# Performance work log

Measured on AMD Instinct MI355X. Metric: run time of the kernel, lower is better.

## Reference

```python
import jax, jax.numpy as jnp
import numpy as np

B, S, D = 4, 2048, 1024
P = 2
N_FEAT = 16          # n_feature_know
N_REST = 16          # n_restore_know
R = 128              # knowledge_rank
D_SPACE = 64


def setup_inputs() -> dict:
    key = jax.random.key(0)
    ks = jax.random.split(key, 6)
    x = jax.random.normal(ks[0], (B, S, D), dtype=jnp.float32)
    # per-token routing weights for each of P feature paths, in [0,1)
    feature_paths = jax.random.uniform(ks[1], (P, B, S, N_FEAT), dtype=jnp.float32)
    f_know = jax.random.normal(ks[2], (N_FEAT, D, R), dtype=jnp.float32) * 0.02
    r_know = jax.random.normal(ks[3], (N_REST, R, D), dtype=jnp.float32) * 0.02
    feature_emb = jax.random.normal(ks[4], (N_FEAT, D_SPACE), dtype=jnp.float32)
    W_router = jax.random.normal(ks[5], (D_SPACE + R, N_REST), dtype=jnp.float32) * 0.05
    return {"x": x, "feature_paths": feature_paths, "f_know": f_know,
            "r_know": r_know, "feature_emb": feature_emb, "W_router": W_router}


def reference(x, feature_paths, f_know, r_know, feature_emb, W_router):
    # Feature projection into all N low-rank banks: [B,S,N,R]
    all_h = jnp.einsum('bsd,ndr->bsnr', x, f_know)
    # Weighted sum over banks per path: [P,B,S,R]
    h_all = jnp.einsum('bsnr,pbsn->pbsr', all_h, feature_paths)
    # Context for restore routing: [P,B,S,D_SPACE]
    neuron_ctx = jnp.einsum('pbsn,nd->pbsd', feature_paths, feature_emb)
    # restore_input = cat([neuron_ctx, h]) -> router -> softmax restore weights
    restore_input = jnp.concatenate([neuron_ctx, h_all], axis=-1)  # [P,B,S,D_SPACE+R]
    logits = jnp.einsum('pbsc,cn->pbsn', restore_input, W_router)
    w = jax.nn.softmax(logits, axis=-1)                            # [P,B,S,N_REST]
    # Restore + per-token weighted combine, summed over P paths: [B,S,D]
    output = jnp.einsum('pbsr,nrd,pbsn->bsd', h_all, r_know, w)
    restore_aux_loss = jnp.float32(0.0)
    return output, restore_aux_loss
```

## Files before the change

### kernel.cpp

```cpp
#include <hip/hip_runtime.h>

typedef __attribute__((ext_vector_type(4))) float f32x4;
typedef __bf16 bf16x8 __attribute__((ext_vector_type(8)));
typedef unsigned short ushort_t;

#define T_TOK 8192
#define DIM   1024
#define NRCOL 2048

#define VMW(n)  asm volatile("s_waitcnt vmcnt(" #n ")" ::: "memory")
#define SB0()   __builtin_amdgcn_sched_barrier(0)
#define BAR()   __builtin_amdgcn_s_barrier()

template<int V> struct IC { static constexpr int value = V; };

static __device__ __forceinline__ unsigned short f2bf(float f) {
  unsigned int u = __builtin_bit_cast(unsigned int, f);
  u += 0x7fffu + ((u >> 16) & 1u);
  return (unsigned short)(u >> 16);
}
static __device__ __forceinline__ float bfbits2f(unsigned int lo16) {
  return __builtin_bit_cast(float, lo16 << 16);
}
static __device__ __forceinline__ void gload16(const void* g, void* l) {
  __builtin_amdgcn_global_load_lds((const __attribute__((address_space(1))) void*)g,
                                   (__attribute__((address_space(3))) void*)l, 16, 0, 0);
}

__global__ __launch_bounds__(256) void cvt_f32_bf16(const float* __restrict__ in,
                                                    unsigned short* __restrict__ out,
                                                    int n4) {
  int i = blockIdx.x * 256 + threadIdx.x;
  const int stride = gridDim.x * 256;
  const float4* in4 = (const float4*)in;
  uint2* o4 = (uint2*)out;
  for (; i < n4; i += stride) {
    float4 v = in4[i];
    uint2 o;
    o.x = (unsigned)f2bf(v.x) | ((unsigned)f2bf(v.y) << 16);
    o.y = (unsigned)f2bf(v.z) | ((unsigned)f2bf(v.w) << 16);
    o4[i] = o;
  }
}

__global__ __launch_bounds__(256) void tcvt(const float* __restrict__ src,
                                            unsigned short* __restrict__ dst,
                                            int rows, int cols,
                                            long sstride, long dstride) {
  src += (size_t)blockIdx.z * sstride;
  dst += (size_t)blockIdx.z * dstride;
  __shared__ float tile[32][33];
  const int tx = threadIdx.x & 31, ty = threadIdx.x >> 5;
  const int r0 = blockIdx.y * 32, c0 = blockIdx.x * 32;
  #pragma unroll
  for (int i = 0; i < 32; i += 8)
    tile[ty + i][tx] = src[(size_t)(r0 + ty + i) * cols + c0 + tx];
  __syncthreads();
  #pragma unroll
  for (int i = 0; i < 32; i += 8)
    dst[(size_t)(c0 + ty + i) * rows + r0 + tx] = f2bf(tile[tx][ty + i]);
}

template<int K, bool OUT_BF16>
__global__ __launch_bounds__(512, 2) void gemmT(const ushort_t* __restrict__ A,
                                                const ushort_t* __restrict__ Bt,
                                                void* __restrict__ Cp, int N) {
  constexpr int nt = K >> 6;
  constexpr int NT3 = (nt + 2) / 3;
  __shared__ ushort_t As[3][256 * 64];
  __shared__ ushort_t Bs[3][128 * 64];
  const int tid = threadIdx.x;
  const int nx = gridDim.x;
  const int orig = blockIdx.y * nx + blockIdx.x;
  const int q = (nx * gridDim.y) >> 3;
  const int swz = (orig & 7) * q + (orig >> 3);
  const int bx = swz % nx, by = swz / nx;

  const int lane = tid & 63, wv = tid >> 6;
  const int wm = wv >> 1, wn = wv & 1;
  const int lrow = lane & 15, lk = lane >> 4;

  const ushort_t* Ab = A + (size_t)by * 256 * K;
  const ushort_t* Bb = Bt + (size_t)bx * 128 * K;

  const int rs = tid >> 3;
  const int cs = (tid & 7) ^ (rs & 7);
  const ushort_t* pA[4];
  const ushort_t* pB[2];
  #pragma unroll
  for (int r = 0; r < 4; ++r) pA[r] = Ab + (size_t)(r * 64 + rs) * K + cs * 8;
  #pragma unroll
  for (int r = 0; r < 2; ++r) pB[r] = Bb + (size_t)(r * 64 + rs) * K + cs * 8;
  const int dA = tid * 8;

  int offA[4][2], offB[4][2];
  #pragma unroll
  for (int m = 0; m < 4; ++m) {
    const int ra = wm * 64 + m * 16 + lrow;
    const int rb = wn * 64 + m * 16 + lrow;
    #pragma unroll
    for (int ks = 0; ks < 2; ++ks) {
      offA[m][ks] = ra * 64 + ((ks * 4 + lk) ^ (ra & 7)) * 8;
      offB[m][ks] = rb * 64 + ((ks * 4 + lk) ^ (rb & 7)) * 8;
    }
  }

  f32x4 acc[4][4];
  #pragma unroll
  for (int m = 0; m < 4; ++m)
    #pragma unroll
    for (int n = 0; n < 4; ++n)
      acc[m][n] = (f32x4){0.f, 0.f, 0.f, 0.f};

  #pragma unroll
  for (int r = 0; r < 4; ++r) gload16(pA[r], (void*)&As[0][r * 4096 + dA]);
  #pragma unroll
  for (int r = 0; r < 2; ++r) gload16(pB[r], (void*)&Bs[0][r * 4096 + dA]);
  #pragma unroll
  for (int r = 0; r < 4; ++r) gload16(pA[r] + 64, (void*)&As[1][r * 4096 + dA]);
  #pragma unroll
  for (int r = 0; r < 2; ++r) gload16(pB[r] + 64, (void*)&Bs[1][r * 4096 + dA]);
  #pragma unroll
  for (int r = 0; r < 4; ++r) pA[r] += 128;
  pB[0] += 128; pB[1] += 128;
  VMW(6); SB0(); BAR(); SB0();

  int t = 0;
  auto body = [&](auto SC) {
    constexpr int S = SC.value;
    constexpr int S2 = (S + 2) % 3;
    if (t >= nt) return;
    bf16x8 av[4][2], bv[4][2];
    #pragma unroll
    for (int m = 0; m < 4; ++m)
      #pragma unroll
      for (int ks = 0; ks < 2; ++ks) {
        av[m][ks] = *(const bf16x8*)&As[S][offA[m][ks]];
        bv[m][ks] = *(const bf16x8*)&Bs[S][offB[m][ks]];
      }
    if (t + 2 < nt) {
      #pragma unroll
      for (int r = 0; r < 4; ++r) gload16(pA[r], (void*)&As[S2][r * 4096 + dA]);
      #pragma unroll
      for (int r = 0; r < 2; ++r) gload16(pB[r], (void*)&Bs[S2][r * 4096 + dA]);
    }
    __builtin_amdgcn_s_setprio(1);
    #pragma unroll
    for (int ks = 0; ks < 2; ++ks)
      #pragma unroll
      for (int m = 0; m < 4; ++m)
        #pragma unroll
        for (int n = 0; n < 4; ++n)
          acc[m][n] = __builtin_amdgcn_mfma_f32_16x16x32_bf16(av[m][ks], bv[n][ks], acc[m][n], 0, 0, 0);
    __builtin_amdgcn_s_setprio(0);
    SB0();
    if (t + 2 < nt) { VMW(6); } else { VMW(0); }
    SB0(); BAR(); SB0();
    #pragma unroll
    for (int r = 0; r < 4; ++r) pA[r] += 64;
    pB[0] += 64; pB[1] += 64;
    ++t;
  };
  #pragma unroll 1
  for (int i = 0; i < NT3; ++i) {
    body(IC<0>{}); body(IC<1>{}); body(IC<2>{});
  }

  #pragma unroll
  for (int m = 0; m < 4; ++m) {
    const int row0 = by * 256 + wm * 64 + m * 16 + lk * 4;
    #pragma unroll
    for (int n = 0; n < 4; ++n) {
      const int col = bx * 128 + wn * 64 + n * 16 + lrow;
      #pragma unroll
      for (int j = 0; j < 4; ++j) {
        const size_t idx = (size_t)(row0 + j) * N + col;
        if constexpr (OUT_BF16) ((ushort_t*)Cp)[idx] = f2bf(acc[m][n][j]);
        else                    ((float*)Cp)[idx] = acc[m][n][j];
      }
    }
  }
}

__global__ __launch_bounds__(256) void middle_kernel(const unsigned short* __restrict__ AH,
                                                     const float* __restrict__ fp,
                                                     const float* __restrict__ femb,
                                                     const float* __restrict__ Wr,
                                                     unsigned short* __restrict__ Mout,
                                                     float* __restrict__ auxout) {
  __shared__ float G[16][16];
  __shared__ float hs[4][2][128];
  __shared__ float wsm[4][2][16];
  const int tid = threadIdx.x;
  {
    const int n = tid >> 4, j = tid & 15;
    float s = 0.f;
    #pragma unroll
    for (int ds = 0; ds < 64; ++ds) s += femb[n * 64 + ds] * Wr[ds * 16 + j];
    G[n][j] = s;
  }
  const int wv = tid >> 6, l = tid & 63;
  const int t = blockIdx.x * 4 + wv;

  float p0[16], p1[16];
  #pragma unroll
  for (int n = 0; n < 16; ++n) {
    p0[n] = fp[t * 16 + n];
    p1[n] = fp[T_TOK * 16 + t * 16 + n];
  }

  float h00 = 0.f, h01 = 0.f, h10 = 0.f, h11 = 0.f;
  const unsigned short* ahrow = AH + (size_t)t * NRCOL;
  #pragma unroll
  for (int n = 0; n < 16; ++n) {
    const unsigned int v = *(const unsigned int*)(ahrow + n * 128 + 2 * l);
    const float a0 = bfbits2f(v & 0xffffu);
    const float a1 = bfbits2f(v >> 16);
    h00 += a0 * p0[n]; h01 += a1 * p0[n];
    h10 += a0 * p1[n]; h11 += a1 * p1[n];
  }
  hs[wv][0][2 * l] = h00; hs[wv][0][2 * l + 1] = h01;
  hs[wv][1][2 * l] = h10; hs[wv][1][2 * l + 1] = h11;
  __syncthreads();

  if (l < 32) {
    const int p = l >> 4, j = l & 15;
    float s = 0.f;
    #pragma unroll
    for (int n = 0; n < 16; ++n) s += (p ? p1[n] : p0[n]) * G[n][j];
    const float* hp = hs[wv][p];
    const float* wr = Wr + 64 * 16 + j;
    float s0 = 0.f, s1 = 0.f, s2 = 0.f, s3 = 0.f;
    #pragma unroll
    for (int r = 0; r < 128; r += 4) {
      s0 += hp[r]     * wr[(r)     * 16];
      s1 += hp[r + 1] * wr[(r + 1) * 16];
      s2 += hp[r + 2] * wr[(r + 2) * 16];
      s3 += hp[r + 3] * wr[(r + 3) * 16];
    }
    s += (s0 + s1) + (s2 + s3);
    float mx = s;
    #pragma unroll
    for (int d = 1; d < 16; d <<= 1) mx = fmaxf(mx, __shfl_xor(mx, d, 64));
    const float e = __expf(s - mx);
    float sum = e;
    #pragma unroll
    for (int d = 1; d < 16; d <<= 1) sum += __shfl_xor(sum, d, 64);
    wsm[wv][p][j] = e / sum;
  }
  __syncthreads();

  unsigned short* mrow = Mout + (size_t)t * NRCOL;
  #pragma unroll
  for (int n = 0; n < 16; ++n) {
    const float w0 = wsm[wv][0][n], w1 = wsm[wv][1][n];
    const float m0 = w0 * h00 + w1 * h10;
    const float m1 = w0 * h01 + w1 * h11;
    const unsigned int pk = (unsigned)f2bf(m0) | ((unsigned)f2bf(m1) << 16);
    *(unsigned int*)(mrow + n * 128 + 2 * l) = pk;
  }
  if (blockIdx.x == 0 && tid == 0) auxout[0] = 0.f;
}

extern "C" void kernel_launch(void* const* d_in, const int* in_sizes, int n_in,
                              void* d_out, int out_size, void* d_ws, size_t ws_size,
                              hipStream_t stream) {
  const float* x    = (const float*)d_in[0];
  const float* fp   = (const float*)d_in[1];
  const float* fk   = (const float*)d_in[2];
  const float* rk   = (const float*)d_in[3];
  const float* femb = (const float*)d_in[4];
  const float* Wr   = (const float*)d_in[5];
  float* out = (float*)d_out;

  char* ws = (char*)d_ws;
  unsigned short* Xbf = (unsigned short*)ws;
  unsigned short* W1t = (unsigned short*)(ws + 16u * 1024 * 1024);
  unsigned short* Mb  = (unsigned short*)ws;
  unsigned short* W2t = (unsigned short*)(ws + 32u * 1024 * 1024);
  unsigned short* AH  = (unsigned short*)(ws + 36u * 1024 * 1024);

  cvt_f32_bf16<<<2048, 256, 0, stream>>>(x, Xbf, (T_TOK * DIM) / 4);
  tcvt<<<dim3(128 / 32, 1024 / 32, 16), 256, 0, stream>>>(fk, W1t, 1024, 128,
                                                          1024L * 128, 128L * 1024);
  tcvt<<<dim3(1024 / 32, 2048 / 32, 1), 256, 0, stream>>>(rk, W2t, 2048, 1024, 0, 0);
  gemmT<1024, true><<<dim3(NRCOL / 128, T_TOK / 256), 512, 0, stream>>>(Xbf, W1t, AH, NRCOL);
  middle_kernel<<<T_TOK / 4, 256, 0, stream>>>(AH, fp, femb, Wr, Mb, out + 8388608);
  gemmT<2048, false><<<dim3(DIM / 128, T_TOK / 256), 512, 0, stream>>>(Mb, W2t, out, DIM);
}
```

Before: 124.4 us.

## Restructure GEMM with parameterized tiles, register double-buffering and split MFMA phases

Replaces the fixed 256x128 GEMM with a templated kernel that takes BM and BK and uses a 256-wide N tile and a 2x4 wave layout. Each k-step is split into two MFMA halves so the LDS fragment reads for the next stage overlap the current compute, and the A fragments are double-buffered in registers. The first GEMM uses 256x256 tiles with BK=32 and the second uses 128x256 tiles with BK=64. This trades more registers, a fully unrolled k-loop and an extra barrier per step for more operand reuse and better overlap of LDS reads with MFMA work.

```diff
diff --git a/kernel.cpp b/kernel.cpp
--- a/kernel.cpp
+++ b/kernel.cpp
@@ -11,8 +11,6 @@
 #define VMW(n)  asm volatile("s_waitcnt vmcnt(" #n ")" ::: "memory")
 #define SB0()   __builtin_amdgcn_sched_barrier(0)
 #define BAR()   __builtin_amdgcn_s_barrier()
-
-template<int V> struct IC { static constexpr int value = V; };
 
 static __device__ __forceinline__ unsigned short f2bf(float f) {
   unsigned int u = __builtin_bit_cast(unsigned int, f);
@@ -61,14 +59,20 @@
     dst[(size_t)(c0 + ty + i) * rows + r0 + tx] = f2bf(tile[tx][ty + i]);
 }
 
-template<int K, bool OUT_BF16>
-__global__ __launch_bounds__(512, 2) void gemmT(const ushort_t* __restrict__ A,
+template<int BM, int BK, int K, bool OUT_BF16>
+__global__ __launch_bounds__(512, 2) void gemmP(const ushort_t* __restrict__ A,
                                                 const ushort_t* __restrict__ Bt,
                                                 void* __restrict__ Cp, int N) {
-  constexpr int nt = K >> 6;
-  constexpr int NT3 = (nt + 2) / 3;
-  __shared__ ushort_t As[3][256 * 64];
-  __shared__ ushort_t Bs[3][128 * 64];
+  constexpr int nt = K / BK;
+  constexpr int KS = BK / 32;
+  constexpr int MF = BM / 32;
+  constexpr int CH = BK / 8;
+  constexpr int AR = BM * BK * 2 / 8192;
+  constexpr int BR = 256 * BK * 2 / 8192;
+  constexpr int LPT = AR + BR;
+  __shared__ ushort_t As[3][BM * BK];
+  __shared__ ushort_t Bs[3][256 * BK];
+
   const int tid = threadIdx.x;
   const int nx = gridDim.x;
   const int orig = blockIdx.y * nx + blockIdx.x;
@@ -77,101 +81,115 @@
   const int bx = swz % nx, by = swz / nx;
 
   const int lane = tid & 63, wv = tid >> 6;
-  const int wm = wv >> 1, wn = wv & 1;
+  const int wm = wv >> 2, wn = wv & 3;
   const int lrow = lane & 15, lk = lane >> 4;
 
-  const ushort_t* Ab = A + (size_t)by * 256 * K;
-  const ushort_t* Bb = Bt + (size_t)bx * 128 * K;
-
-  const int rs = tid >> 3;
-  const int cs = (tid & 7) ^ (rs & 7);
-  const ushort_t* pA[4];
-  const ushort_t* pB[2];
-  #pragma unroll
-  for (int r = 0; r < 4; ++r) pA[r] = Ab + (size_t)(r * 64 + rs) * K + cs * 8;
-  #pragma unroll
-  for (int r = 0; r < 2; ++r) pB[r] = Bb + (size_t)(r * 64 + rs) * K + cs * 8;
-  const int dA = tid * 8;
-
-  int offA[4][2], offB[4][2];
-  #pragma unroll
-  for (int m = 0; m < 4; ++m) {
-    const int ra = wm * 64 + m * 16 + lrow;
-    const int rb = wn * 64 + m * 16 + lrow;
-    #pragma unroll
-    for (int ks = 0; ks < 2; ++ks) {
-      offA[m][ks] = ra * 64 + ((ks * 4 + lk) ^ (ra & 7)) * 8;
-      offB[m][ks] = rb * 64 + ((ks * 4 + lk) ^ (rb & 7)) * 8;
-    }
-  }
-
-  f32x4 acc[4][4];
-  #pragma unroll
-  for (int m = 0; m < 4; ++m)
+  const ushort_t* Ab = A + (size_t)by * BM * K;
+  const ushort_t* Bb = Bt + (size_t)bx * 256 * K;
+
+  const int srow = tid * 16 / (BK * 2);
+  const int sch = ((tid * 16 >> 4) & (CH - 1)) ^ (srow & (CH - 1));
+  constexpr int RPR = 8192 / (BK * 2);
+  const ushort_t* pA[AR];
+  const ushort_t* pB[BR];
+  #pragma unroll
+  for (int r = 0; r < AR; ++r) pA[r] = Ab + (size_t)(r * RPR + srow) * K + sch * 8;
+  #pragma unroll
+  for (int r = 0; r < BR; ++r) pB[r] = Bb + (size_t)(r * RPR + srow) * K + sch * 8;
+  const int dL = tid * 8;
+
+  int oA[MF], oB[4];
+  #pragma unroll
+  for (int m = 0; m < MF; ++m) {
+    const int r = wm * (BM / 2) + m * 16 + lrow;
+    oA[m] = r * BK + (lk ^ (r & (CH - 1))) * 8;
+  }
+  #pragma unroll
+  for (int n = 0; n < 4; ++n) {
+    const int r = wn * 64 + n * 16 + lrow;
+    oB[n] = r * BK + (lk ^ (r & (CH - 1))) * 8;
+  }
+
+  f32x4 acc[MF][4];
+  #pragma unroll
+  for (int m = 0; m < MF; ++m)
     #pragma unroll
     for (int n = 0; n < 4; ++n)
       acc[m][n] = (f32x4){0.f, 0.f, 0.f, 0.f};
 
-  #pragma unroll
-  for (int r = 0; r < 4; ++r) gload16(pA[r], (void*)&As[0][r * 4096 + dA]);
-  #pragma unroll
-  for (int r = 0; r < 2; ++r) gload16(pB[r], (void*)&Bs[0][r * 4096 + dA]);
-  #pragma unroll
-  for (int r = 0; r < 4; ++r) gload16(pA[r] + 64, (void*)&As[1][r * 4096 + dA]);
-  #pragma unroll
-  for (int r = 0; r < 2; ++r) gload16(pB[r] + 64, (void*)&Bs[1][r * 4096 + dA]);
-  #pragma unroll
-  for (int r = 0; r < 4; ++r) pA[r] += 128;
-  pB[0] += 128; pB[1] += 128;
-  VMW(6); SB0(); BAR(); SB0();
-
-  int t = 0;
-  auto body = [&](auto SC) {
-    constexpr int S = SC.value;
-    constexpr int S2 = (S + 2) % 3;
-    if (t >= nt) return;
-    bf16x8 av[4][2], bv[4][2];
-    #pragma unroll
-    for (int m = 0; m < 4; ++m)
-      #pragma unroll
-      for (int ks = 0; ks < 2; ++ks) {
-        av[m][ks] = *(const bf16x8*)&As[S][offA[m][ks]];
-        bv[m][ks] = *(const bf16x8*)&Bs[S][offB[m][ks]];
-      }
-    if (t + 2 < nt) {
-      #pragma unroll
-      for (int r = 0; r < 4; ++r) gload16(pA[r], (void*)&As[S2][r * 4096 + dA]);
-      #pragma unroll
-      for (int r = 0; r < 2; ++r) gload16(pB[r], (void*)&Bs[S2][r * 4096 + dA]);
+  auto stage = [&](int s, int adv) {
+    #pragma unroll
+    for (int r = 0; r < AR; ++r) gload16(pA[r] + adv, (void*)&As[s][r * 4096 + dL]);
+    #pragma unroll
+    for (int r = 0; r < BR; ++r) gload16(pB[r] + adv, (void*)&Bs[s][r * 4096 + dL]);
+  };
+
+  stage(0, 0);
+  stage(1, BK);
+  if constexpr (LPT == 4) VMW(4); else VMW(6);
+  SB0(); BAR(); SB0();
+
+  bf16x8 av[2][MF][KS], bv01[2][KS], bv23[2][KS];
+  #pragma unroll
+  for (int m = 0; m < MF; ++m)
+    #pragma unroll
+    for (int ks = 0; ks < KS; ++ks)
+      av[0][m][ks] = *(const bf16x8*)&As[0][oA[m] ^ (ks * 32)];
+  #pragma unroll
+  for (int n = 0; n < 2; ++n)
+    #pragma unroll
+    for (int ks = 0; ks < KS; ++ks)
+      bv01[n][ks] = *(const bf16x8*)&Bs[0][oB[n] ^ (ks * 32)];
+
+  #pragma unroll
+  for (int t = 0; t < nt; ++t) {
+    const int s = t % 3, s1 = (t + 1) % 3, s2 = (t + 2) % 3;
+    const int p = t & 1;
+    if (t + 2 < nt) stage(s2, (t + 2) * BK);
+    #pragma unroll
+    for (int n = 0; n < 2; ++n)
+      #pragma unroll
+      for (int ks = 0; ks < KS; ++ks)
+        bv23[n][ks] = *(const bf16x8*)&Bs[s][oB[n + 2] ^ (ks * 32)];
+    #pragma unroll
+    for (int ks = 0; ks < KS; ++ks)
+      #pragma unroll
+      for (int m = 0; m < MF; ++m)
+        #pragma unroll
+        for (int n = 0; n < 2; ++n)
+          acc[m][n] = __builtin_amdgcn_mfma_f32_16x16x32_bf16(av[p][m][ks], bv01[n][ks], acc[m][n], 0, 0, 0);
+    SB0();
+    if (t + 2 < nt) { if constexpr (LPT == 4) VMW(4); else VMW(6); }
+    else            { VMW(0); }
+    BAR(); SB0();
+    if (t + 1 < nt) {
+      #pragma unroll
+      for (int m = 0; m < MF; ++m)
+        #pragma unroll
+        for (int ks = 0; ks < KS; ++ks)
+          av[p ^ 1][m][ks] = *(const bf16x8*)&As[s1][oA[m] ^ (ks * 32)];
+      #pragma unroll
+      for (int n = 0; n < 2; ++n)
+        #pragma unroll
+        for (int ks = 0; ks < KS; ++ks)
+          bv01[n][ks] = *(const bf16x8*)&Bs[s1][oB[n] ^ (ks * 32)];
     }
-    __builtin_amdgcn_s_setprio(1);
-    #pragma unroll
-    for (int ks = 0; ks < 2; ++ks)
-      #pragma unroll
-      for (int m = 0; m < 4; ++m)
+    #pragma unroll
+    for (int ks = 0; ks < KS; ++ks)
+      #pragma unroll
+      for (int m = 0; m < MF; ++m)
         #pragma unroll
-        for (int n = 0; n < 4; ++n)
-          acc[m][n] = __builtin_amdgcn_mfma_f32_16x16x32_bf16(av[m][ks], bv[n][ks], acc[m][n], 0, 0, 0);
-    __builtin_amdgcn_s_setprio(0);
-    SB0();
-    if (t + 2 < nt) { VMW(6); } else { VMW(0); }
+        for (int n = 0; n < 2; ++n)
+          acc[m][n + 2] = __builtin_amdgcn_mfma_f32_16x16x32_bf16(av[p][m][ks], bv23[n][ks], acc[m][n + 2], 0, 0, 0);
     SB0(); BAR(); SB0();
-    #pragma unroll
-    for (int r = 0; r < 4; ++r) pA[r] += 64;
-    pB[0] += 64; pB[1] += 64;
-    ++t;
-  };
-  #pragma unroll 1
-  for (int i = 0; i < NT3; ++i) {
-    body(IC<0>{}); body(IC<1>{}); body(IC<2>{});
-  }
-
-  #pragma unroll
-  for (int m = 0; m < 4; ++m) {
-    const int row0 = by * 256 + wm * 64 + m * 16 + lk * 4;
+  }
+
+  #pragma unroll
+  for (int m = 0; m < MF; ++m) {
+    const int row0 = by * BM + wm * (BM / 2) + m * 16 + lk * 4;
     #pragma unroll
     for (int n = 0; n < 4; ++n) {
-      const int col = bx * 128 + wn * 64 + n * 16 + lrow;
+      const int col = bx * 256 + wn * 64 + n * 16 + lrow;
       #pragma unroll
       for (int j = 0; j < 4; ++j) {
         const size_t idx = (size_t)(row0 + j) * N + col;
@@ -284,7 +302,7 @@
   tcvt<<<dim3(128 / 32, 1024 / 32, 16), 256, 0, stream>>>(fk, W1t, 1024, 128,
                                                           1024L * 128, 128L * 1024);
   tcvt<<<dim3(1024 / 32, 2048 / 32, 1), 256, 0, stream>>>(rk, W2t, 2048, 1024, 0, 0);
-  gemmT<1024, true><<<dim3(NRCOL / 128, T_TOK / 256), 512, 0, stream>>>(Xbf, W1t, AH, NRCOL);
+  gemmP<256, 32, 1024, true><<<dim3(NRCOL / 256, T_TOK / 256), 512, 0, stream>>>(Xbf, W1t, AH, NRCOL);
   middle_kernel<<<T_TOK / 4, 256, 0, stream>>>(AH, fp, femb, Wr, Mb, out + 8388608);
-  gemmT<2048, false><<<dim3(DIM / 128, T_TOK / 256), 512, 0, stream>>>(Mb, W2t, out, DIM);
-}
+  gemmP<128, 64, 2048, false><<<dim3(DIM / 256, T_TOK / 128), 512, 0, stream>>>(Mb, W2t, out, DIM);
+}
```

After: 115.9 us. 6.9% less time.

## Switch GEMMs to 32x32x16 MFMA with 128x256 tiles and full unrolling

Applied to the files above, without the earlier changes.

Rewrites the bf16 GEMM kernel to use 32x32x16 MFMA instructions instead of 16x16x32, with a 128x256 block tile (A rows x B rows) and a 2x4 wave layout where each wave computes 64x64 from 2x2 MFMA tiles. The K loop is fully unrolled with compile-time stage indices, and the LDS swizzle is adapted to the new fragment layout. The larger MFMA shape needs fewer LDS fragment reads per flop and fewer instructions, at the cost of more register pressure from full unrolling and a different, more strided store pattern in the epilogue.

```diff
diff --git a/kernel.cpp b/kernel.cpp
--- a/kernel.cpp
+++ b/kernel.cpp
@@ -1,6 +1,6 @@
 #include <hip/hip_runtime.h>
 
-typedef __attribute__((ext_vector_type(4))) float f32x4;
+typedef __attribute__((ext_vector_type(16))) float f32x16;
 typedef __bf16 bf16x8 __attribute__((ext_vector_type(8)));
 typedef unsigned short ushort_t;
 
@@ -11,8 +11,6 @@
 #define VMW(n)  asm volatile("s_waitcnt vmcnt(" #n ")" ::: "memory")
 #define SB0()   __builtin_amdgcn_sched_barrier(0)
 #define BAR()   __builtin_amdgcn_s_barrier()
-
-template<int V> struct IC { static constexpr int value = V; };
 
 static __device__ __forceinline__ unsigned short f2bf(float f) {
   unsigned int u = __builtin_bit_cast(unsigned int, f);
@@ -62,13 +60,13 @@
 }
 
 template<int K, bool OUT_BF16>
-__global__ __launch_bounds__(512, 2) void gemmT(const ushort_t* __restrict__ A,
-                                                const ushort_t* __restrict__ Bt,
-                                                void* __restrict__ Cp, int N) {
-  constexpr int nt = K >> 6;
-  constexpr int NT3 = (nt + 2) / 3;
-  __shared__ ushort_t As[3][256 * 64];
-  __shared__ ushort_t Bs[3][128 * 64];
+__global__ __launch_bounds__(512, 2) void gemm32(const ushort_t* __restrict__ A,
+                                                 const ushort_t* __restrict__ Bt,
+                                                 void* __restrict__ Cp, int N) {
+  constexpr int nt = K / 64;
+  __shared__ ushort_t As[3][128 * 64];
+  __shared__ ushort_t Bs[3][256 * 64];
+
   const int tid = threadIdx.x;
   const int nx = gridDim.x;
   const int orig = blockIdx.y * nx + blockIdx.x;
@@ -77,104 +75,92 @@
   const int bx = swz % nx, by = swz / nx;
 
   const int lane = tid & 63, wv = tid >> 6;
-  const int wm = wv >> 1, wn = wv & 1;
-  const int lrow = lane & 15, lk = lane >> 4;
-
-  const ushort_t* Ab = A + (size_t)by * 256 * K;
-  const ushort_t* Bb = Bt + (size_t)bx * 128 * K;
-
-  const int rs = tid >> 3;
-  const int cs = (tid & 7) ^ (rs & 7);
-  const ushort_t* pA[4];
-  const ushort_t* pB[2];
-  #pragma unroll
-  for (int r = 0; r < 4; ++r) pA[r] = Ab + (size_t)(r * 64 + rs) * K + cs * 8;
-  #pragma unroll
-  for (int r = 0; r < 2; ++r) pB[r] = Bb + (size_t)(r * 64 + rs) * K + cs * 8;
-  const int dA = tid * 8;
-
-  int offA[4][2], offB[4][2];
-  #pragma unroll
-  for (int m = 0; m < 4; ++m) {
-    const int ra = wm * 64 + m * 16 + lrow;
-    const int rb = wn * 64 + m * 16 + lrow;
-    #pragma unroll
-    for (int ks = 0; ks < 2; ++ks) {
-      offA[m][ks] = ra * 64 + ((ks * 4 + lk) ^ (ra & 7)) * 8;
-      offB[m][ks] = rb * 64 + ((ks * 4 + lk) ^ (rb & 7)) * 8;
-    }
-  }
-
-  f32x4 acc[4][4];
-  #pragma unroll
-  for (int m = 0; m < 4; ++m)
-    #pragma unroll
-    for (int n = 0; n < 4; ++n)
-      acc[m][n] = (f32x4){0.f, 0.f, 0.f, 0.f};
-
-  #pragma unroll
-  for (int r = 0; r < 4; ++r) gload16(pA[r], (void*)&As[0][r * 4096 + dA]);
-  #pragma unroll
-  for (int r = 0; r < 2; ++r) gload16(pB[r], (void*)&Bs[0][r * 4096 + dA]);
-  #pragma unroll
-  for (int r = 0; r < 4; ++r) gload16(pA[r] + 64, (void*)&As[1][r * 4096 + dA]);
-  #pragma unroll
-  for (int r = 0; r < 2; ++r) gload16(pB[r] + 64, (void*)&Bs[1][r * 4096 + dA]);
-  #pragma unroll
-  for (int r = 0; r < 4; ++r) pA[r] += 128;
-  pB[0] += 128; pB[1] += 128;
+  const int wm = wv >> 2, wn = wv & 3;
+  const int l31 = lane & 31, hi = lane >> 5;
+
+  const ushort_t* Ab = A + (size_t)by * 128 * K;
+  const ushort_t* Bb = Bt + (size_t)bx * 256 * K;
+
+  const int srow = tid >> 3;
+  const int sch = (tid & 7) ^ (srow & 7);
+  const ushort_t* pA[2];
+  const ushort_t* pB[4];
+  #pragma unroll
+  for (int r = 0; r < 2; ++r) pA[r] = Ab + (size_t)(r * 64 + srow) * K + sch * 8;
+  #pragma unroll
+  for (int r = 0; r < 4; ++r) pB[r] = Bb + (size_t)(r * 64 + srow) * K + sch * 8;
+  const int dL = tid * 8;
+
+  auto stage = [&](int s, int adv) {
+    #pragma unroll
+    for (int r = 0; r < 2; ++r) gload16(pA[r] + adv, (void*)&As[s][r * 4096 + dL]);
+    #pragma unroll
+    for (int r = 0; r < 4; ++r) gload16(pB[r] + adv, (void*)&Bs[s][r * 4096 + dL]);
+  };
+
+  int oA[2], oB[2];
+  #pragma unroll
+  for (int m = 0; m < 2; ++m) {
+    const int r = wm * 64 + m * 32 + l31;
+    oA[m] = r * 64 + (hi ^ (r & 7)) * 8;
+  }
+  #pragma unroll
+  for (int n = 0; n < 2; ++n) {
+    const int r = wn * 64 + n * 32 + l31;
+    oB[n] = r * 64 + (hi ^ (r & 7)) * 8;
+  }
+
+  f32x16 acc[2][2];
+  #pragma unroll
+  for (int m = 0; m < 2; ++m)
+    #pragma unroll
+    for (int n = 0; n < 2; ++n)
+      #pragma unroll
+      for (int j = 0; j < 16; ++j) acc[m][n][j] = 0.f;
+
+  stage(0, 0);
+  stage(1, 64);
   VMW(6); SB0(); BAR(); SB0();
 
-  int t = 0;
-  auto body = [&](auto SC) {
-    constexpr int S = SC.value;
-    constexpr int S2 = (S + 2) % 3;
-    if (t >= nt) return;
-    bf16x8 av[4][2], bv[4][2];
-    #pragma unroll
-    for (int m = 0; m < 4; ++m)
-      #pragma unroll
-      for (int ks = 0; ks < 2; ++ks) {
-        av[m][ks] = *(const bf16x8*)&As[S][offA[m][ks]];
-        bv[m][ks] = *(const bf16x8*)&Bs[S][offB[m][ks]];
-      }
-    if (t + 2 < nt) {
-      #pragma unroll
-      for (int r = 0; r < 4; ++r) gload16(pA[r], (void*)&As[S2][r * 4096 + dA]);
-      #pragma unroll
-      for (int r = 0; r < 2; ++r) gload16(pB[r], (void*)&Bs[S2][r * 4096 + dA]);
-    }
+  #pragma unroll
+  for (int t = 0; t < nt; ++t) {
+    const int s = t % 3, s2 = (t + 2) % 3;
+    bf16x8 av[2][4], bv[2][4];
+    #pragma unroll
+    for (int m = 0; m < 2; ++m)
+      #pragma unroll
+      for (int ks = 0; ks < 4; ++ks)
+        av[m][ks] = *(const bf16x8*)&As[s][oA[m] ^ (ks * 16)];
+    #pragma unroll
+    for (int n = 0; n < 2; ++n)
+      #pragma unroll
+      for (int ks = 0; ks < 4; ++ks)
+        bv[n][ks] = *(const bf16x8*)&Bs[s][oB[n] ^ (ks * 16)];
+    if (t + 2 < nt) stage(s2, (t + 2) * 64);
     __builtin_amdgcn_s_setprio(1);
     #pragma unroll
-    for (int ks = 0; ks < 2; ++ks)
-      #pragma unroll
-      for (int m = 0; m < 4; ++m)
+    for (int ks = 0; ks < 4; ++ks)
+      #pragma unroll
+      for (int m = 0; m < 2; ++m)
         #pragma unroll
-        for (int n = 0; n < 4; ++n)
-          acc[m][n] = __builtin_amdgcn_mfma_f32_16x16x32_bf16(av[m][ks], bv[n][ks], acc[m][n], 0, 0, 0);
+        for (int n = 0; n < 2; ++n)
+          acc[m][n] = __builtin_amdgcn_mfma_f32_32x32x16_bf16(av[m][ks], bv[n][ks], acc[m][n], 0, 0, 0);
     __builtin_amdgcn_s_setprio(0);
     SB0();
     if (t + 2 < nt) { VMW(6); } else { VMW(0); }
     SB0(); BAR(); SB0();
-    #pragma unroll
-    for (int r = 0; r < 4; ++r) pA[r] += 64;
-    pB[0] += 64; pB[1] += 64;
-    ++t;
-  };
-  #pragma unroll 1
-  for (int i = 0; i < NT3; ++i) {
-    body(IC<0>{}); body(IC<1>{}); body(IC<2>{});
-  }
-
-  #pragma unroll
-  for (int m = 0; m < 4; ++m) {
-    const int row0 = by * 256 + wm * 64 + m * 16 + lk * 4;
-    #pragma unroll
-    for (int n = 0; n < 4; ++n) {
-      const int col = bx * 128 + wn * 64 + n * 16 + lrow;
-      #pragma unroll
-      for (int j = 0; j < 4; ++j) {
-        const size_t idx = (size_t)(row0 + j) * N + col;
+  }
+
+  #pragma unroll
+  for (int m = 0; m < 2; ++m) {
+    const int row0 = by * 128 + wm * 64 + m * 32 + 4 * hi;
+    #pragma unroll
+    for (int n = 0; n < 2; ++n) {
+      const int col = bx * 256 + wn * 64 + n * 32 + l31;
+      #pragma unroll
+      for (int j = 0; j < 16; ++j) {
+        const int grow = row0 + (j & 3) + 8 * (j >> 2);
+        const size_t idx = (size_t)grow * N + col;
         if constexpr (OUT_BF16) ((ushort_t*)Cp)[idx] = f2bf(acc[m][n][j]);
         else                    ((float*)Cp)[idx] = acc[m][n][j];
       }
@@ -284,7 +270,7 @@
   tcvt<<<dim3(128 / 32, 1024 / 32, 16), 256, 0, stream>>>(fk, W1t, 1024, 128,
                                                           1024L * 128, 128L * 1024);
   tcvt<<<dim3(1024 / 32, 2048 / 32, 1), 256, 0, stream>>>(rk, W2t, 2048, 1024, 0, 0);
-  gemmT<1024, true><<<dim3(NRCOL / 128, T_TOK / 256), 512, 0, stream>>>(Xbf, W1t, AH, NRCOL);
+  gemm32<1024, true><<<dim3(NRCOL / 256, T_TOK / 128), 512, 0, stream>>>(Xbf, W1t, AH, NRCOL);
   middle_kernel<<<T_TOK / 4, 256, 0, stream>>>(AH, fp, femb, Wr, Mb, out + 8388608);
-  gemmT<2048, false><<<dim3(DIM / 128, T_TOK / 256), 512, 0, stream>>>(Mb, W2t, out, DIM);
-}
+  gemm32<2048, false><<<dim3(DIM / 256, T_TOK / 128), 512, 0, stream>>>(Mb, W2t, out, DIM);
+}
```

Result: no change. 126.4 us (+1.6%).
